# Performance work log

Measured on AMD Instinct MI355X. Metric: run time of the kernel, lower is better.

Reference implementation:

```python
import jax, jax.numpy as jnp
import numpy as np

WIN = 15
BINS = 32
ALPHA = 0.9
LAM1 = 0.5
LAM2 = 0.5


def _tmedian(x, axis):
    # torch-style median: k-th smallest with k=(n-1)//2 (lower middle), keepdims
    n = x.shape[axis]
    s = jnp.sort(x, axis=axis)
    return jnp.take(s, jnp.array([(n - 1) // 2]), axis=axis)


def _box_sum_1d(x, k, axis):
    # sliding-window sum (zero padding) via cumsum / integral image
    p = k // 2
    L = x.shape[axis]
    c = jnp.cumsum(x, axis=axis)
    pad = [(0, 0)] * x.ndim
    pad[axis] = (1, 0)
    c = jnp.pad(c, pad)
    i = jnp.arange(L)
    hi = jnp.clip(i + p + 1, 0, L)
    lo = jnp.clip(i - p, 0, L)
    return jnp.take(c, hi, axis=axis) - jnp.take(c, lo, axis=axis)


def _counts_1d(L, k, dtype):
    p = k // 2
    i = jnp.arange(L)
    return (jnp.clip(i + p + 1, 0, L) - jnp.clip(i - p, 0, L)).astype(dtype)


def box_avg(x, k):
    # avg_pool2d(stride=1, padding=k//2, count_include_pad=False) on [B,C,H,W]
    s = _box_sum_1d(_box_sum_1d(x, k, 2), k, 3)
    c = _counts_1d(x.shape[2], k, x.dtype)[:, None] * _counts_1d(x.shape[3], k, x.dtype)[None, :]
    return s / c


def avg3(x):
    # avg_pool2d(k=3, stride=1, pad=1, count_include_pad=True)
    return _box_sum_1d(_box_sum_1d(x, 3, 2), 3, 3) / 9.0


def _softplus(x):
    t = jnp.log1p(jnp.exp(-jnp.abs(x)))
    return jnp.where(x >= 0, x + t, t)


def _conv3(x, k):
    return jax.lax.conv_general_dilated(x, k, (1, 1), ((1, 1), (1, 1)),
                                        dimension_numbers=('NCHW', 'OIHW', 'NCHW'))


def _forward(lab, a_rand):
    B, _, H, W = lab.shape
    N = H * W
    f32 = lab.dtype
    L = lab[:, 0:1]
    a = lab[:, 1:2]
    b = lab[:, 2:3]
    kx = jnp.array([[-1, 0, 1], [-2, 0, 2], [-1, 0, 1]], f32).reshape(1, 1, 3, 3)
    ky = jnp.array([[-1, -2, -1], [0, 0, 0], [1, 2, 1]], f32).reshape(1, 1, 3, 3)
    gx = _conv3(L, kx)
    gy = _conv3(L, ky)
    E = avg3(gx * gx) + avg3(gy * gy)           # structure-tensor trace
    S = jnp.sqrt(a * a + b * b + 1e-8)           # chroma
    Xf = jnp.concatenate([E, S], 1).reshape(B, 2, N).transpose(0, 2, 1)   # [B,N,2]
    yf = L.reshape(B, 1, N).transpose(0, 2, 1)                            # [B,N,1]
    XtX = jnp.einsum('bni,bnj->bij', Xf, Xf)
    XtY = jnp.einsum('bni,bnj->bij', Xf, yf)
    beta = jnp.linalg.solve(XtX + 1e-6 * jnp.eye(2, dtype=f32), XtY)[..., 0]  # [B,2]
    pred = beta[:, 0][:, None, None, None] * E + beta[:, 1][:, None, None, None] * S
    L_perp = L - pred
    # robust scale + whitening of [L_perp, E, S]
    X3f = jnp.concatenate([L_perp, E, S], 1).reshape(B, 3, N).transpose(0, 2, 1)  # [B,N,3]
    med = _tmedian(X3f, 1)
    mad = _tmedian(jnp.abs(X3f - med), 1) * 1.4826 + 1e-8
    Xz = (X3f - med) / mad
    diff = Xz - Xz.mean(1, keepdims=True)
    cov = jnp.einsum('bni,bnj->bij', diff, diff) / N
    e, V = jnp.linalg.eigh(jnp.maximum(cov, 1e-8))
    Wwh = jnp.einsum('bij,bj,bkj->bik', V, 1.0 / jnp.sqrt(e), V)
    Xw = diff @ Wwh                                                       # [B,N,3]
    # 128-way random-projection kurtosis search
    an = a_rand / (jnp.linalg.norm(a_rand, axis=-1, keepdims=True) + 1e-12)
    z = jnp.einsum('bni,bti->bnt', Xw, an)                                # [B,N,128]
    zc = z - z.mean(1, keepdims=True)
    m2 = (zc ** 2).mean(1) + 1e-12
    m4 = (zc ** 4).mean(1)
    kurt = m4 / (m2 * m2) - 3.0
    best = jnp.argmax(jnp.abs(kurt), axis=1)
    a_star = jnp.take_along_axis(an, best[:, None, None], axis=1)[:, 0]   # [B,3]
    z_best = jnp.einsum('bni,bi->bn', Xw, a_star)                         # [B,N]
    # 1-D 2-component GMM, 10 EM steps
    K = 2
    q25 = jnp.quantile(z_best, 0.25, axis=1)
    q75 = jnp.quantile(z_best, 0.75, axis=1)
    mu = jnp.stack([q25, q75], 1)[:, None, :]   # [B,1,K]
    var = jnp.ones((B, 1, K), f32)
    pi = jnp.full((B, 1, K), 0.5, f32)
    x1 = z_best[:, :, None]                      # [B,N,1]
    R = jnp.zeros((B, N, K), f32)
    for _ in range(10):
        logp = (-0.5 * ((x1 - mu) ** 2 / (var + 1e-6))
                - 0.5 * jnp.log(var + 1e-6) + jnp.log(pi + 1e-8))
        R = jnp.exp(jax.nn.log_softmax(logp, axis=2))
        Nk = R.sum(1, keepdims=True)             # [B,1,K]
        mu = (R * x1).sum(1, keepdims=True) / (Nk + 1e-8)
        var = (R * (x1 - mu) ** 2).sum(1, keepdims=True) / (Nk + 1e-8) + 1e-6
        pi = Nk / N
    R_alpha = R ** ALPHA
    R_alpha = R_alpha / (R_alpha.sum(2, keepdims=True) + 1e-8)
    rk_maps = R_alpha.transpose(0, 2, 1).reshape(B, K, 1, H, W)
    # per-cluster weighted Mahalanobis distance in [L_perp,E,S] space
    eye3 = jnp.eye(3, dtype=f32)
    Dk = []
    for k in range(K):
        w = R_alpha[:, :, k]
        Wsum = w.sum(1, keepdims=True) + 1e-8
        mu_k = jnp.einsum('bn,bni->bi', w, X3f) / Wsum
        Xm = X3f - mu_k[:, None, :]
        cov_k = jnp.einsum('bn,bni,bnj->bij', w, Xm, Xm) / Wsum[..., None] + 1e-6 * eye3
        inv_k = jnp.linalg.inv(cov_k)
        Dk.append(jnp.sqrt(jnp.einsum('bni,bij,bnj->bn', Xm, inv_k, Xm) + 1e-8))
    Dk = jnp.stack(Dk, 2)                        # [B,N,K]
    Rtemp = jax.nn.softmax(jnp.log(R_alpha + 1e-8), axis=2)
    D_M = (Rtemp * Dk).sum(2).reshape(B, 1, H, W)
    # local luminance anomaly (box-filtered weighted mean/std)
    Z_LLA = []
    for k in range(K):
        rk = rk_maps[:, k]
        den = box_avg(rk, WIN) + 1e-8
        mu_b = box_avg(rk * L_perp, WIN) / den
        var_b = jnp.maximum(box_avg(rk * L_perp ** 2, WIN) / den - mu_b ** 2, 1e-8)
        lla = jnp.abs(L_perp - mu_b) / (jnp.sqrt(var_b) + 1e-8)
        v = lla.reshape(B, 1, N)
        mv = _tmedian(v, 2)
        mdv = _tmedian(jnp.abs(v - mv), 2) * 1.4826 + 1e-8
        Z_LLA.append(((v - mv) / mdv).reshape(B, 1, H, W))
    # global-vs-local histogram distance (GLD)
    Lmin = L_perp.min(axis=(2, 3), keepdims=True)
    Lmax = L_perp.max(axis=(2, 3), keepdims=True)
    Lnorm = jnp.clip((L_perp - Lmin) / (Lmax - Lmin + 1e-8), 0, 1)
    idx = jnp.clip((Lnorm * BINS).astype(jnp.int32), 0, BINS - 1)[:, 0]   # [B,H,W]
    onehot = jax.nn.one_hot(idx, BINS, dtype=f32).transpose(0, 3, 1, 2)   # [B,bins,H,W]
    Z_GLD = []
    for k in range(K):
        rk = rk_maps[:, k]
        w_hist = onehot * rk
        g_hist = w_hist.reshape(B, BINS, N).sum(-1)
        g_hist = g_hist / (g_hist.sum(1, keepdims=True) + 1e-8)
        g_cdf = jnp.cumsum(g_hist, 1)
        loc_cdf = jnp.cumsum(box_avg(w_hist, WIN), 1) / (box_avg(rk, WIN) + 1e-8)
        GLD = jnp.abs(loc_cdf - g_cdf[:, :, None, None]).sum(1) / BINS    # [B,H,W]
        v = GLD.reshape(B, N)
        mv = _tmedian(v, 1)                                              # [B,1]
        mdv = _tmedian(jnp.abs(v - mv), 1) * 1.4826 + 1e-8
        Z_GLD.append(((GLD - mv[:, :, None]) / mdv[:, :, None])[:, None])
    gamma = jnp.ones_like(L_perp)
    for k in range(K):
        gamma = gamma + rk_maps[:, k] * (LAM1 * _softplus(Z_LLA[k]) + LAM2 * _softplus(Z_GLD[k]))
    # structural decorrelation term over [E,S]
    ES = jnp.concatenate([E, S], 1).reshape(B, 2, N).transpose(0, 2, 1)
    med2 = _tmedian(ES, 1)
    mad2 = _tmedian(jnp.abs(ES - med2), 1) * 1.4826 + 1e-8
    ESz = (ES - med2) / mad2
    d = ESz - ESz.mean(1, keepdims=True)
    cov2 = jnp.einsum('bni,bnj->bij', d, d) / N + 1e-6 * jnp.eye(2, dtype=f32)
    inv2 = jnp.linalg.inv(cov2)
    d2 = jnp.einsum('bni,bij,bnj->bn', d, inv2, d).reshape(B, 1, H, W)
    R_struct = jnp.exp(-0.5 * d2)
    L_anom = jnp.maximum(D_M * gamma * (1.0 - R_struct), 0.0)
    flat = L_anom.reshape(B, -1)
    q1 = jnp.quantile(flat, 0.01, axis=1).reshape(B, 1, 1, 1)
    q9 = jnp.quantile(flat, 0.99, axis=1).reshape(B, 1, 1, 1)
    L_anom_norm = jnp.clip((L_anom - q1) / (q9 - q1 + 1e-8), 0, 1)
    return L_perp, L_anom_norm


def setup_inputs() -> dict:
    key = jax.random.key(0)
    k1, k2 = jax.random.split(key)
    return {
        'batch_lab_raw': jax.random.normal(k1, (2, 3, 384, 384), jnp.float32),
        'a_rand': jax.random.normal(k2, (2, 128, 3), jnp.float32),
    }


def reference(batch_lab_raw, a_rand):
    return _forward(batch_lab_raw, a_rand)
```

## Files before the change

kernel.cpp:

```cpp
#include <hip/hip_runtime.h>
#include <math.h>

#define HH 384
#define WW 384
#define NPIX (HH*WW)
#define NB 2
#define BN (NB*NPIX)
#define NT 128
#define NBINS 32
#define MEDRANK ((NPIX-1)/2)
#define RB 72
#define RB2 288
#define SEL_BLK 64
#define KDG 8
#define KSEG 16

#define A_BETA 0
#define A_XZ   16
#define A_ES   40
#define A_DK   56
#define A_GMM  128
#define A_ZTOT 272
#define A_GHIST 288
#define A_KURT 512

#define F_BETA 0
#define F_X3   8
#define F_MEAN 24
#define F_WWH  32
#define F_ASTAR 828
#define F_ZBQ  868
#define F_DKINV 880
#define F_CM   918
#define F_ESI  940
#define F_LAQ  952
#define F_GCDF 968
#define F_MMS_MIN 1280
#define F_MMS_MAX 1408


__device__ __forceinline__ double waveSum(double v){
#pragma unroll
  for(int o=32;o;o>>=1) v += __shfl_down(v,o,64);
  return v;
}
__device__ __forceinline__ unsigned f2u(float f){
  unsigned u = __float_as_uint(f);
  return (u & 0x80000000u) ? ~u : (u | 0x80000000u);
}
__device__ __forceinline__ float u2f(unsigned u){
  return __uint_as_float((u & 0x80000000u) ? (u ^ 0x80000000u) : ~u);
}
__device__ __forceinline__ float sp(float x){
  float t = log1pf(expf(-fabsf(x)));
  return x >= 0.f ? x + t : t;
}

struct SelBatch {
  const float* src[8];
  int rank[8];
  int fslot[8];
  int nt;
  int medmad;
};

__device__ void pickN(const unsigned* hp, int nb, int rank, unsigned& sel, int& nrank){
  __shared__ unsigned s_cum[256];
  __shared__ unsigned s_res[2];
  int tid = threadIdx.x;
  int base = tid*8;
  unsigned loc[8]; unsigned tsum=0;
#pragma unroll
  for(int j=0;j<8;j++){ unsigned v=(base+j<nb)?hp[base+j]:0u; loc[j]=v; tsum+=v; }
  s_cum[tid]=tsum;
  __syncthreads();
  for(int o=1;o<256;o<<=1){
    unsigned t=(tid>=o)?s_cum[tid-o]:0u;
    __syncthreads();
    s_cum[tid]+=t;
    __syncthreads();
  }
  unsigned cum=s_cum[tid], ex=cum-tsum;
  if(tsum>0u && (unsigned)rank>=ex && (unsigned)rank<cum){
    int rr=rank-(int)ex; unsigned bsel=0;
#pragma unroll
    for(int j=0;j<8;j++){ if((unsigned)rr<loc[j]){ bsel=(unsigned)(base+j); break; } rr-=(int)loc[j]; }
    s_res[0]=bsel; s_res[1]=(unsigned)rr;
  }
  __syncthreads();
  sel=s_res[0]; nrank=(int)s_res[1];
  __syncthreads();
}

__global__ void k_zero(double* A, float* F, unsigned* T, unsigned* H){
  int i = blockIdx.x*256 + threadIdx.x;
  if(i < 2048) A[i] = 0.0;
  if(i < 4096){
    unsigned* U = (unsigned*)F;
    unsigned v = 0u;
    if(i>=F_MMS_MIN && i<F_MMS_MIN+64) v = 0xFFFFFFFFu;
    U[i] = v;
  }
  if(i < 512) T[i] = 0u;
  for(int j=i; j<240*2048; j+=65536) H[j]=0u;
}

__global__ __launch_bounds__(256) void k_selp(SelBatch sb, unsigned* Hh, unsigned* T,
                                              float* F, int bid, int stage, int p){
  int task = blockIdx.x / SEL_BLK;
  int blk  = blockIdx.x % SEL_BLK;
  unsigned* meta = T + 384 + task*8;
  float center = (stage==1) ? __uint_as_float(meta[4]) : 0.f;
  unsigned pre = (p==2) ? 0u : meta[stage*2];
  __shared__ unsigned lh[2048];
  for(int j=threadIdx.x;j<2048;j+=256) lh[j]=0u;
  __syncthreads();
  const float* src = sb.src[task];
  for(int i=blk*256+threadIdx.x; i<NPIX; i+=SEL_BLK*256){
    float v = src[i];
    if(stage) v = fabsf(v-center);
    unsigned u = f2u(v);
    unsigned bin; bool ok;
    if(p==2){ bin = u>>21; ok = true; }
    else if(p==1){ bin = (u>>10)&2047u; ok = ((u>>21)==pre); }
    else { bin = u&1023u; ok = ((u>>10)==pre); }
    if(ok) atomicAdd(&lh[bin],1u);
  }
  __syncthreads();
  unsigned* hp = Hh + (size_t)(((bid*8+task)*2+stage)*3 + (2-p))*2048;
  for(int j=threadIdx.x;j<2048;j+=256){ unsigned c=lh[j]; if(c) atomicAdd(hp+j,c); }
  __shared__ int s_last;
  __syncthreads();
  if(threadIdx.x==0){
    __threadfence();
    s_last = (atomicAdd(&T[16+bid*64+task*8+stage*4+(2-p)],1u) == (unsigned)(SEL_BLK-1));
  }
  __syncthreads();
  if(!s_last) return;
  int r = (p==2) ? sb.rank[task] : (int)meta[stage*2+1];
  int nb = (p==0) ? 1024 : 2048;
  unsigned sel; int nr;
  pickN(hp, nb, r, sel, nr);
  if(threadIdx.x==0){
    if(p==2){ meta[stage*2]=sel; meta[stage*2+1]=(unsigned)nr; }
    else if(p==1){ meta[stage*2]=(pre<<11)|sel; meta[stage*2+1]=(unsigned)nr; }
    else {
      float val = u2f((pre<<10)|sel);
      if(stage==0){
        if(sb.medmad) meta[4]=__float_as_uint(val);
        else F[sb.fslot[task]]=val;
      } else {
        F[sb.fslot[task]]   = __uint_as_float(meta[4]);
        F[sb.fslot[task]+1] = val*1.4826f + 1e-8f;
      }
    }
  }
}

__device__ void quad_from_stats(double N0,double Sx0,double Sxx0,double Sxt,double Sxxt,
                                float& qa,float& qb,float& qc){
  double Nt=(double)NPIX;
  double N1=Nt-N0, Sx1=Sxt-Sx0, Sxx1=Sxxt-Sxx0;
  double mu0=Sx0/(N0+1e-8), mu1=Sx1/(N1+1e-8);
  double v0=(Sxx0-2.0*mu0*Sx0+mu0*mu0*N0)/(N0+1e-8)+1e-6;
  double v1=(Sxx1-2.0*mu1*Sx1+mu1*mu1*N1)/(N1+1e-8)+1e-6;
  double p0=N0/Nt, p1=N1/Nt;
  double c0=-0.5*log(v0+1e-6)+log(p0+1e-8);
  double c1=-0.5*log(v1+1e-6)+log(p1+1e-8);
  double iv0=0.5/(v0+1e-6), iv1=0.5/(v1+1e-6);
  qa=(float)(iv0-iv1);
  qb=(float)(2.0*(iv1*mu1-iv0*mu0));
  qc=(float)(iv0*mu0*mu0-iv1*mu1*mu1+c1-c0);
}
__device__ void quad_init(const float* F,int b,float& qa,float& qb,float& qc){
  const float* z = F + F_ZBQ + b*4;
  double h25 = 0.25*(double)(NPIX-1); double f25 = h25 - floor(h25);
  double h75 = 0.75*(double)(NPIX-1); double f75 = h75 - floor(h75);
  double mu0 = (double)z[0] + f25*((double)z[1]-(double)z[0]);
  double mu1 = (double)z[2] + f75*((double)z[3]-(double)z[2]);
  double iv = 0.5/(1.0+1e-6);
  qa = 0.f;
  qb = (float)(2.0*iv*(mu1-mu0));
  qc = (float)(iv*(mu0*mu0-mu1*mu1));
}

__global__ __launch_bounds__(256) void k_sobel(const float* lab, float* S, float* E){
  int bx = blockIdx.x % 24, by = (blockIdx.x/24) % 24, b = blockIdx.x/576;
  __shared__ float Lt[20][21];
  __shared__ float G[18][19];
  const float* Lb = lab + b*3*NPIX;
  int ox = bx*16, oy = by*16;
  for(int i=threadIdx.x; i<400; i+=256){
    int lx=i%20, ly=i/20;
    int gx_=ox-2+lx, gy_=oy-2+ly;
    Lt[ly][lx] = (gx_<0||gx_>=WW||gy_<0||gy_>=HH)?0.f:Lb[gy_*WW+gx_];
  }
  __syncthreads();
  for(int i=threadIdx.x; i<324; i+=256){
    int lx=i%18, ly=i/18;
    int px=lx+1, py=ly+1;
    int gxp=ox-2+px, gyp=oy-2+py;
    float g=0.f;
    if(gxp>=0&&gxp<WW&&gyp>=0&&gyp<HH){
      float gx = -Lt[py-1][px-1]+Lt[py-1][px+1] -2.f*Lt[py][px-1]+2.f*Lt[py][px+1] -Lt[py+1][px-1]+Lt[py+1][px+1];
      float gy = -Lt[py-1][px-1]-2.f*Lt[py-1][px]-Lt[py-1][px+1] +Lt[py+1][px-1]+2.f*Lt[py+1][px]+Lt[py+1][px+1];
      g = gx*gx+gy*gy;
    }
    G[ly][lx]=g;
  }
  __syncthreads();
  int tx = threadIdx.x%16, ty = threadIdx.x/16;
  float s=0;
#pragma unroll
  for(int dy=0;dy<3;dy++)
#pragma unroll
    for(int dx=0;dx<3;dx++) s += G[ty+dy][tx+dx];
  int n = (oy+ty)*WW + ox+tx;
  E[b*NPIX+n] = s*(1.f/9.f);
  float av=Lb[NPIX+n], bv=Lb[2*NPIX+n];
  S[b*NPIX+n] = sqrtf(av*av+bv*bv+1e-8f);
}

__global__ void k_beta_red(const float* E,const float* S,const float* lab,double* A,
                           float* F, unsigned* T){
  int b = blockIdx.x / RB, blk = blockIdx.x % RB;
  double s[5]={0,0,0,0,0};
  for(int n = blk*256 + threadIdx.x; n < NPIX; n += RB*256){
    float e=E[b*NPIX+n], ss=S[b*NPIX+n], l=lab[b*3*NPIX+n];
    s[0]+=(double)e*e; s[1]+=(double)e*ss; s[2]+=(double)ss*ss;
    s[3]+=(double)e*l; s[4]+=(double)ss*l;
  }
  __shared__ double red[4][5];
  int wave=threadIdx.x>>6, lane=threadIdx.x&63;
#pragma unroll
  for(int q=0;q<5;q++){
    s[q]=waveSum(s[q]);
    if(lane==0) red[wave][q]=s[q];
  }
  __syncthreads();
  if(threadIdx.x<5){
    double v = red[0][threadIdx.x]+red[1][threadIdx.x]+red[2][threadIdx.x]+red[3][threadIdx.x];
    atomicAdd(&A[A_BETA+b*5+threadIdx.x], v);
  }
  __shared__ int s_last;
  __syncthreads();
  if(threadIdx.x==0){
    __threadfence();
    s_last = (atomicAdd(&T[0],1u) == (unsigned)(NB*RB-1));
  }
  __syncthreads();
  if(!s_last || threadIdx.x) return;
  for(int bb=0;bb<NB;bb++){
    double EE=A[A_BETA+bb*5],ES=A[A_BETA+bb*5+1],SS=A[A_BETA+bb*5+2],EL=A[A_BETA+bb*5+3],SL=A[A_BETA+bb*5+4];
    double a00=EE+1e-6, a01=ES, a11=SS+1e-6;
    double det=a00*a11-a01*a01;
    F[F_BETA+bb*2]  =(float)(( a11*EL - a01*SL)/det);
    F[F_BETA+bb*2+1]=(float)((-a01*EL + a00*SL)/det);
  }
}

__global__ void k_lperp(const float* lab,const float* E,const float* S,const float* F,float* out0){
  int i = blockIdx.x*256 + threadIdx.x;
  int b=i/NPIX, n=i%NPIX;
  float v = lab[b*3*NPIX+n] - F[F_BETA+b*2]*E[i] - F[F_BETA+b*2+1]*S[i];
  out0[i] = v;
  unsigned u = f2u(v);
  unsigned mn=u, mx=u;
#pragma unroll
  for(int o=32;o;o>>=1){
    unsigned a = __shfl_down(mn,o,64); mn = (a<mn)?a:mn;
    unsigned c = __shfl_down(mx,o,64); mx = (c>mx)?c:mx;
  }
  __shared__ unsigned rmn[4], rmx[4];
  int wave=threadIdx.x>>6, lane=threadIdx.x&63;
  if(lane==0){ rmn[wave]=mn; rmx[wave]=mx; }
  __syncthreads();
  if(threadIdx.x==0){
    unsigned m0 = rmn[0]; unsigned m1 = rmx[0];
    for(int w=1;w<4;w++){ if(rmn[w]<m0)m0=rmn[w]; if(rmx[w]>m1)m1=rmx[w]; }
    unsigned* U = (unsigned*)F;
    int slot = blockIdx.x & 31;
    atomicMin(&U[F_MMS_MIN+b*32+slot], m0);
    atomicMax(&U[F_MMS_MAX+b*32+slot], m1);
  }
}

__global__ void k_xz_red(const float* Lp,const float* E,const float* S,float* F,double* A,
                         unsigned* T){
  int b = blockIdx.x / RB, blk = blockIdx.x % RB;
  const float* M = F + F_X3 + b*6;
  double s[9]={0,0,0,0,0,0,0,0,0};
  for(int n = blk*256 + threadIdx.x; n < NPIX; n += RB*256){
    float z0=(Lp[b*NPIX+n]-M[0])/M[1];
    float z1=(E [b*NPIX+n]-M[2])/M[3];
    float z2=(S [b*NPIX+n]-M[4])/M[5];
    s[0]+=z0; s[1]+=z1; s[2]+=z2;
    s[3]+=(double)z0*z0; s[4]+=(double)z0*z1; s[5]+=(double)z0*z2;
    s[6]+=(double)z1*z1; s[7]+=(double)z1*z2; s[8]+=(double)z2*z2;
  }
  __shared__ double red[4][9];
  int wave=threadIdx.x>>6, lane=threadIdx.x&63;
#pragma unroll
  for(int q=0;q<9;q++){
    s[q]=waveSum(s[q]);
    if(lane==0) red[wave][q]=s[q];
  }
  __syncthreads();
  if(threadIdx.x<9){
    double v = red[0][threadIdx.x]+red[1][threadIdx.x]+red[2][threadIdx.x]+red[3][threadIdx.x];
    atomicAdd(&A[A_XZ+b*9+threadIdx.x], v);
  }
  __shared__ int s_last;
  __syncthreads();
  if(threadIdx.x==0){
    __threadfence();
    s_last = (atomicAdd(&T[1],1u) == (unsigned)(NB*RB-1));
  }
  __syncthreads();
  if(!s_last) return;
  int bb = threadIdx.x;
  if(bb>=NB) return;
  const double* ss = A + A_XZ + bb*9;
  double inv = 1.0/(double)NPIX;
  double m0=ss[0]*inv, m1=ss[1]*inv, m2=ss[2]*inv;
  double a[3][3];
  a[0][0]=fmax(ss[3]*inv-m0*m0,1e-8);
  a[0][1]=a[1][0]=fmax(ss[4]*inv-m0*m1,1e-8);
  a[0][2]=a[2][0]=fmax(ss[5]*inv-m0*m2,1e-8);
  a[1][1]=fmax(ss[6]*inv-m1*m1,1e-8);
  a[1][2]=a[2][1]=fmax(ss[7]*inv-m1*m2,1e-8);
  a[2][2]=fmax(ss[8]*inv-m2*m2,1e-8);
  double V[3][3]={{1,0,0},{0,1,0},{0,0,1}};
  for(int sweep=0;sweep<40;sweep++){
    for(int pp=0;pp<3;pp++){
      int p = (pp==2)?1:0;
      int q = (pp==0)?1:2;
      double apq=a[p][q];
      if(fabs(apq)<1e-30) continue;
      double theta=(a[q][q]-a[p][p])/(2.0*apq);
      double t=((theta>=0)?1.0:-1.0)/(fabs(theta)+sqrt(1.0+theta*theta));
      double c=1.0/sqrt(1.0+t*t), sn=t*c;
      for(int k2=0;k2<3;k2++){ double akp=a[k2][p],akq=a[k2][q];
        a[k2][p]=c*akp-sn*akq; a[k2][q]=sn*akp+c*akq; }
      for(int k2=0;k2<3;k2++){ double apk=a[p][k2],aqk=a[q][k2];
        a[p][k2]=c*apk-sn*aqk; a[q][k2]=sn*apk+c*aqk; }
      for(int k2=0;k2<3;k2++){ double vkp=V[k2][p],vkq=V[k2][q];
        V[k2][p]=c*vkp-sn*vkq; V[k2][q]=sn*vkp+c*vkq; }
    }
  }
  double is0=1.0/sqrt(a[0][0]), is1=1.0/sqrt(a[1][1]), is2=1.0/sqrt(a[2][2]);
  for(int i=0;i<3;i++) for(int j=0;j<3;j++){
    double w = V[i][0]*is0*V[j][0] + V[i][1]*is1*V[j][1] + V[i][2]*is2*V[j][2];
    F[F_WWH + bb*9 + i*3 + j] = (float)w;
  }
  F[F_MEAN+bb*3]=(float)m0; F[F_MEAN+bb*3+1]=(float)m1; F[F_MEAN+bb*3+2]=(float)m2;
}

__global__ void k_xw(const float* Lp,const float* E,const float* S,const float* F,
                     float* Xw,int* idxP){
  __shared__ float s_mn, s_mx;
  int i = blockIdx.x*256 + threadIdx.x;
  int b=i/NPIX;
  if(threadIdx.x==0){
    const unsigned* U = (const unsigned*)F;
    unsigned mn=0xFFFFFFFFu, mx=0u;
    for(int s2=0;s2<32;s2++){
      unsigned a=U[F_MMS_MIN+b*32+s2]; if(a<mn)mn=a;
      unsigned c=U[F_MMS_MAX+b*32+s2]; if(c>mx)mx=c;
    }
    s_mn=u2f(mn); s_mx=u2f(mx);
  }
  __syncthreads();
  const float* M = F + F_X3 + b*6;
  float lp = Lp[i];
  float z0=(lp-M[0])/M[1];
  float z1=(E [i]-M[2])/M[3];
  float z2=(S [i]-M[4])/M[5];
  float d0=z0-F[F_MEAN+b*3], d1=z1-F[F_MEAN+b*3+1], d2=z2-F[F_MEAN+b*3+2];
  const float* Wm = F + F_WWH + b*9;
  Xw[3*(size_t)i  ]=d0*Wm[0]+d1*Wm[3]+d2*Wm[6];
  Xw[3*(size_t)i+1]=d0*Wm[1]+d1*Wm[4]+d2*Wm[7];
  Xw[3*(size_t)i+2]=d0*Wm[2]+d1*Wm[5]+d2*Wm[8];
  float ln = (lp-s_mn)/(s_mx-s_mn+1e-8f);
  ln = fminf(fmaxf(ln,0.f),1.f);
  int id = (int)(ln*32.f);
  idxP[i] = id>31?31:(id<0?0:id);
}

__global__ __launch_bounds__(256) void k_kurt(const float* Xw, const float* arand,
                                              double* A, float* F, unsigned* T){
  int g = blockIdx.x;
  int b   = g / ((NT/KDG)*KSEG);
  int rem = g % ((NT/KDG)*KSEG);
  int dg  = rem / KSEG;
  int seg = rem % KSEG;
  float a0[KDG],a1[KDG],a2[KDG];
#pragma unroll
  for(int j=0;j<KDG;j++){
    const float* ar = arand + (b*NT+dg*KDG+j)*3;
    float q0=ar[0],q1=ar[1],q2=ar[2];
    float nrm=(float)(sqrt((double)q0*q0+(double)q1*q1+(double)q2*q2)+1e-12);
    a0[j]=q0/nrm; a1[j]=q1/nrm; a2[j]=q2/nrm;
  }
  const float* X = Xw + (size_t)b*NPIX*3;
  double s[KDG][4];
#pragma unroll
  for(int j=0;j<KDG;j++){ s[j][0]=0; s[j][1]=0; s[j][2]=0; s[j][3]=0; }
  const int cnt = NPIX/KSEG;
  int start = seg*cnt;
  for(int n=start+threadIdx.x; n<start+cnt; n+=256){
    const float* p = X + 3*(size_t)n;
    float x=p[0], y=p[1], z=p[2];
#pragma unroll
    for(int j=0;j<KDG;j++){
      float zz = fmaf(x,a0[j],fmaf(y,a1[j], z*a2[j]));
      float z2f = zz*zz;
      s[j][0]+=zz; s[j][1]+=z2f; s[j][2]+=z2f*zz; s[j][3]+=(double)z2f*z2f;
    }
  }
  __shared__ double red[4][KDG*4];
  int wave=threadIdx.x>>6, lane=threadIdx.x&63;
#pragma unroll
  for(int j=0;j<KDG;j++)
#pragma unroll
    for(int m=0;m<4;m++){
      double v=waveSum(s[j][m]);
      if(lane==0) red[wave][j*4+m]=v;
    }
  __syncthreads();
  if(threadIdx.x<KDG*4){
    double v = red[0][threadIdx.x]+red[1][threadIdx.x]+red[2][threadIdx.x]+red[3][threadIdx.x];
    int j=threadIdx.x>>2, m=threadIdx.x&3;
    atomicAdd(&A[A_KURT + (size_t)(b*NT+dg*KDG+j)*4 + m], v);
  }
  __shared__ int s_last;
  __syncthreads();
  if(threadIdx.x==0){
    __threadfence();
    s_last = (atomicAdd(&T[5],1u) == (unsigned)(NB*(NT/KDG)*KSEG-1));
  }
  __syncthreads();
  if(!s_last) return;
  __shared__ float ak[NB*NT];
  {
    int tid=threadIdx.x;
    const double* K = A + A_KURT + (size_t)tid*4;
    double inv=1.0/(double)NPIX;
    double mean=K[0]*inv, M2=K[1]*inv, M3=K[2]*inv, M4=K[3]*inv;
    double m2 = M2 - mean*mean + 1e-12;
    double m4 = M4 - 4.0*mean*M3 + 6.0*mean*mean*M2 - 3.0*mean*mean*mean*mean;
    ak[tid] = (float)fabs(m4/(m2*m2) - 3.0);
  }
  __syncthreads();
  if(threadIdx.x<NB){
    int bb=threadIdx.x;
    int best=0; float bv=ak[bb*NT];
    for(int j=1;j<NT;j++){ float v=ak[bb*NT+j]; if(v>bv){bv=v;best=j;} }
    const float* ar = arand + (bb*NT+best)*3;
    double nrm = sqrt((double)ar[0]*ar[0]+(double)ar[1]*ar[1]+(double)ar[2]*ar[2])+1e-12;
    F[F_ASTAR+bb*3]  =(float)(ar[0]/nrm);
    F[F_ASTAR+bb*3+1]=(float)(ar[1]/nrm);
    F[F_ASTAR+bb*3+2]=(float)(ar[2]/nrm);
  }
}

__global__ void k_zbest(const float* Xw,const float* F,float* zb,double* A){
  int i = blockIdx.x*256 + threadIdx.x;
  int b=i/NPIX;
  const float* p = Xw + 3*(size_t)i;
  float v = p[0]*F[F_ASTAR+b*3] + p[1]*F[F_ASTAR+b*3+1] + p[2]*F[F_ASTAR+b*3+2];
  zb[i]=v;
  double s0=waveSum((double)v), s1=waveSum((double)v*v);
  __shared__ double red[4][2];
  int wave=threadIdx.x>>6, lane=threadIdx.x&63;
  if(lane==0){ red[wave][0]=s0; red[wave][1]=s1; }
  __syncthreads();
  if(threadIdx.x<2){
    double v2 = red[0][threadIdx.x]+red[1][threadIdx.x]+red[2][threadIdx.x]+red[3][threadIdx.x];
    atomicAdd(&A[A_ZTOT+b*2+threadIdx.x], v2);
  }
}

__global__ __launch_bounds__(256) void k_gmm_red(const float* zb, const float* F, double* A, int it){
  __shared__ float Q[3];
  __shared__ double red[4][3];
  int b = blockIdx.x / RB2, blk = blockIdx.x % RB2;
  if(threadIdx.x==0){
    float qa,qb,qc;
    if(it==0) quad_init(F,b,qa,qb,qc);
    else {
      const double* g = A + A_GMM + (it-1)*8 + b*4;
      quad_from_stats(g[0],g[1],g[2],A[A_ZTOT+b*2],A[A_ZTOT+b*2+1],qa,qb,qc);
    }
    Q[0]=qa;Q[1]=qb;Q[2]=qc;
  }
  __syncthreads();
  float qa=Q[0],qb=Q[1],qc=Q[2];
  double s0=0,s1=0,s2=0;
  for(int n = blk*256 + threadIdx.x; n < NPIX; n += RB2*256){
    float x = zb[b*NPIX+n];
    float f = fmaf(fmaf(qa,x,qb),x,qc);
    float r0 = 1.f/(1.f+expf(f));
    float rx = r0*x;
    s0+=r0; s1+=rx; s2+=(double)rx*x;
  }
  int wave=threadIdx.x>>6, lane=threadIdx.x&63;
  s0=waveSum(s0); s1=waveSum(s1); s2=waveSum(s2);
  if(lane==0){ red[wave][0]=s0; red[wave][1]=s1; red[wave][2]=s2; }
  __syncthreads();
  if(threadIdx.x<3){
    double v = red[0][threadIdx.x]+red[1][threadIdx.x]+red[2][threadIdx.x]+red[3][threadIdx.x];
    atomicAdd(&A[A_GMM+it*8+b*4+threadIdx.x], v);
  }
}

__global__ void k_ralpha(const float* zb, float* F, double* A, const int* idxP,
                         float* Ra0, float* Ra1, unsigned* T){
  __shared__ float h0[NBINS], h1[NBINS];
  __shared__ float Q[3];
  if(threadIdx.x<NBINS){ h0[threadIdx.x]=0.f; h1[threadIdx.x]=0.f; }
  int i = blockIdx.x*256 + threadIdx.x;
  int b=i/NPIX;
  if(threadIdx.x==0){
    const double* g = A + A_GMM + 8*8 + b*4;
    float qa,qb,qc;
    quad_from_stats(g[0],g[1],g[2],A[A_ZTOT+b*2],A[A_ZTOT+b*2+1],qa,qb,qc);
    Q[0]=qa;Q[1]=qb;Q[2]=qc;
  }
  __syncthreads();
  float x = zb[i];
  float f = fmaf(fmaf(Q[0],x,Q[1]),x,Q[2]);
  float r0 = 1.f/(1.f+expf(f));
  float r1 = 1.f-r0;
  float ra0=powf(r0,0.9f), ra1=powf(r1,0.9f);
  float s=ra0+ra1+1e-8f;
  ra0/=s; ra1/=s;
  Ra0[i]=ra0; Ra1[i]=ra1;
  int id = idxP[i];
  atomicAdd(&h0[id], ra0);
  atomicAdd(&h1[id], ra1);
  __syncthreads();
  if(threadIdx.x<NBINS){
    if(h0[threadIdx.x]!=0.f) atomicAdd(&A[A_GHIST+(0*NB+b)*32+threadIdx.x], (double)h0[threadIdx.x]);
    if(h1[threadIdx.x]!=0.f) atomicAdd(&A[A_GHIST+(1*NB+b)*32+threadIdx.x], (double)h1[threadIdx.x]);
  }
  __shared__ int s_last;
  __syncthreads();
  if(threadIdx.x==0){
    __threadfence();
    s_last = (atomicAdd(&T[2],1u) == (unsigned)(BN/256-1));
  }
  __syncthreads();
  if(!s_last) return;
  int t = threadIdx.x;
  if(t>=4) return;
  const double* gh = A + A_GHIST + t*32;
  double sum=0;
  for(int j=0;j<NBINS;j++) sum += gh[j];
  double c=0;
  for(int j=0;j<NBINS;j++){
    c += gh[j]/(sum+1e-8);
    F[F_GCDF+t*32+j]=(float)c;
  }
}

__global__ void k_dk_red(const float* Lp,const float* E,const float* S,
                         const float* Ra0,const float* Ra1,double* A,float* F,unsigned* T){
  int b = blockIdx.x / RB, blk = blockIdx.x % RB;
  double s[20];
#pragma unroll
  for(int q=0;q<20;q++) s[q]=0;
  for(int n = blk*256 + threadIdx.x; n < NPIX; n += RB*256){
    int i=b*NPIX+n;
    double w0=Ra0[i], w1=Ra1[i];
    double x0=Lp[i], x1=E[i], x2=S[i];
    s[0]+=w0; s[1]+=w0*x0; s[2]+=w0*x1; s[3]+=w0*x2;
    s[4]+=w0*x0*x0; s[5]+=w0*x0*x1; s[6]+=w0*x0*x2; s[7]+=w0*x1*x1; s[8]+=w0*x1*x2; s[9]+=w0*x2*x2;
    s[10]+=w1; s[11]+=w1*x0; s[12]+=w1*x1; s[13]+=w1*x2;
    s[14]+=w1*x0*x0; s[15]+=w1*x0*x1; s[16]+=w1*x0*x2; s[17]+=w1*x1*x1; s[18]+=w1*x1*x2; s[19]+=w1*x2*x2;
  }
  __shared__ double red[4][20];
  int wave=threadIdx.x>>6, lane=threadIdx.x&63;
#pragma unroll
  for(int q=0;q<20;q++){
    s[q]=waveSum(s[q]);
    if(lane==0) red[wave][q]=s[q];
  }
  __syncthreads();
  if(threadIdx.x<20){
    double v = red[0][threadIdx.x]+red[1][threadIdx.x]+red[2][threadIdx.x]+red[3][threadIdx.x];
    atomicAdd(&A[A_DK+b*20+threadIdx.x], v);
  }
  __shared__ int s_last;
  __syncthreads();
  if(threadIdx.x==0){
    __threadfence();
    s_last = (atomicAdd(&T[3],1u) == (unsigned)(NB*RB-1));
  }
  __syncthreads();
  if(!s_last || threadIdx.x) return;
  for(int bb=0;bb<NB;bb++) for(int k=0;k<2;k++){
    const double* ss = A + A_DK + (bb*2+k)*10;
    double W0=ss[0], Ws=W0+1e-8;
    double mu0=ss[1]/Ws, mu1=ss[2]/Ws, mu2=ss[3]/Ws;
    double C00=(ss[4]-2.0*mu0*ss[1]+mu0*mu0*W0)/Ws + 1e-6;
    double C01=(ss[5]-mu0*ss[2]-mu1*ss[1]+mu0*mu1*W0)/Ws;
    double C02=(ss[6]-mu0*ss[3]-mu2*ss[1]+mu0*mu2*W0)/Ws;
    double C11=(ss[7]-2.0*mu1*ss[2]+mu1*mu1*W0)/Ws + 1e-6;
    double C12=(ss[8]-mu1*ss[3]-mu2*ss[2]+mu1*mu2*W0)/Ws;
    double C22=(ss[9]-2.0*mu2*ss[3]+mu2*mu2*W0)/Ws + 1e-6;
    double det = C00*(C11*C22-C12*C12) - C01*(C01*C22-C12*C02) + C02*(C01*C12-C11*C02);
    double id = 1.0/det;
    float* P = F + F_DKINV + (bb*2+k)*9;
    P[0]=(float)((C11*C22-C12*C12)*id);
    P[1]=(float)((C02*C12-C01*C22)*id);
    P[2]=(float)((C01*C12-C02*C11)*id);
    P[3]=(float)((C00*C22-C02*C02)*id);
    P[4]=(float)((C01*C02-C00*C12)*id);
    P[5]=(float)((C00*C11-C01*C01)*id);
    P[6]=(float)mu0; P[7]=(float)mu1; P[8]=(float)mu2;
  }
}
__global__ void k_dm(const float* Lp,const float* E,const float* S,
                     const float* Ra0,const float* Ra1,const float* F,float* DM){
  int i = blockIdx.x*256 + threadIdx.x; if(i>=BN) return;
  int b=i/NPIX;
  float x0=Lp[i], x1=E[i], x2=S[i];
  float D[2];
#pragma unroll
  for(int k=0;k<2;k++){
    const float* P = F + F_DKINV + (b*2+k)*9;
    float d0=x0-P[6], d1=x1-P[7], d2=x2-P[8];
    float q = d0*d0*P[0] + d1*d1*P[3] + d2*d2*P[5]
            + 2.f*(d0*d1*P[1] + d0*d2*P[2] + d1*d2*P[4]);
    D[k]=sqrtf(q+1e-8f);
  }
  float w0=Ra0[i]+1e-8f, w1=Ra1[i]+1e-8f;
  DM[i] = (w0*D[0]+w1*D[1])/(w0+w1);
}

__global__ __launch_bounds__(256) void k_lla(const float* Ra0, const float* Ra1,
                                             const float* Lp, float* tmpL){
  int kk = blockIdx.x / (NB*576);
  int inner = blockIdx.x % (NB*576);
  int bx = inner % 24, by = (inner/24) % 24, b = inner/576;
  const float* rk = kk ? Ra1 : Ra0;
  __shared__ float Rt[30][31], Lt[30][31];
  __shared__ float h0[30][17], h1[30][17], h2[30][17];
  int ox = bx*16, oy = by*16;
  const float* Rb = rk + (size_t)b*NPIX;
  const float* Lb = Lp + (size_t)b*NPIX;
  for(int i=threadIdx.x; i<900; i+=256){
    int lx=i%30, ly=i/30;
    int gx_=ox-7+lx, gy_=oy-7+ly;
    bool in = (gx_>=0&&gx_<WW&&gy_>=0&&gy_<HH);
    Rt[ly][lx]= in ? Rb[gy_*WW+gx_] : 0.f;
    Lt[ly][lx]= in ? Lb[gy_*WW+gx_] : 0.f;
  }
  __syncthreads();
  for(int i=threadIdx.x; i<480; i+=256){
    int j=i%16, r=i/16;
    float s0=0,s1=0,s2=0;
#pragma unroll
    for(int d=0;d<15;d++){
      float rr=Rt[r][j+d], ll=Lt[r][j+d];
      s0+=rr; float rl=rr*ll; s1+=rl; s2+=rl*ll;
    }
    h0[r][j]=s0; h1[r][j]=s1; h2[r][j]=s2;
  }
  __syncthreads();
  int tx=threadIdx.x%16, ty=threadIdx.x/16;
  float S0=0,S1=0,S2=0;
#pragma unroll
  for(int d=0;d<15;d++){ S0+=h0[ty+d][tx]; S1+=h1[ty+d][tx]; S2+=h2[ty+d][tx]; }
  int x=ox+tx, y=oy+ty;
  float cy = (float)((y+8<HH?y+8:HH)-(y-7>0?y-7:0));
  float cx = (float)((x+8<WW?x+8:WW)-(x-7>0?x-7:0));
  float cnt = cy*cx;
  float den = S0/cnt + 1e-8f;
  float mu  = (S1/cnt)/den;
  float var = fmaxf((S2/cnt)/den - mu*mu, 1e-8f);
  int n = y*WW+x;
  tmpL[(size_t)kk*BN + b*NPIX+n] = fabsf(Lb[n]-mu)/(sqrtf(var)+1e-8f);
}

__global__ __launch_bounds__(256) void k_gldf(const float* Ra0, const float* Ra1,
                                              const int* idxP, const float* F, float* tmpG){
  int kk = blockIdx.x / (NB*576);
  int inner = blockIdx.x % (NB*576);
  int bx = inner % 24, by = (inner/24) % 24, b = inner/576;
  const float* rk = kk ? Ra1 : Ra0;
  __shared__ float Rt[30][31];
  __shared__ unsigned char It[30][32];
  __shared__ float Hh[32*480];
  __shared__ float gc[NBINS];
  if(threadIdx.x<NBINS) gc[threadIdx.x]=F[F_GCDF+(kk*NB+b)*32+threadIdx.x];
  int ox=bx*16, oy=by*16;
  const float* Rb = rk + (size_t)b*NPIX;
  const int* Ib = idxP + (size_t)b*NPIX;
  for(int i=threadIdx.x;i<900;i+=256){
    int lx=i%30, ly=i/30;
    int gx_=ox-7+lx, gy_=oy-7+ly;
    bool in = (gx_>=0&&gx_<WW&&gy_>=0&&gy_<HH);
    Rt[ly][lx] = in? Rb[gy_*WW+gx_] : 0.f;
    It[ly][lx] = in? (unsigned char)Ib[gy_*WW+gx_] : 0;
  }
  for(int i=threadIdx.x;i<32*480;i+=256) Hh[i]=0.f;
  __syncthreads();
  for(int i=threadIdx.x;i<480;i+=256){
    int j=i%16, r=i/16;
    for(int d=0;d<15;d++) Hh[(int)It[r][j+d]*480 + i] += Rt[r][j+d];
  }
  __syncthreads();
  int tx=threadIdx.x%16, ty=threadIdx.x/16;
  float vs[32];
  float tot=0;
#pragma unroll
  for(int bin=0;bin<NBINS;bin++){
    float s=0;
#pragma unroll
    for(int d=0;d<15;d++) s += Hh[bin*480 + (ty+d)*16+tx];
    vs[bin]=s; tot+=s;
  }
  int x=ox+tx, y=oy+ty;
  float cy = (float)((y+8<HH?y+8:HH)-(y-7>0?y-7:0));
  float cx = (float)((x+8<WW?x+8:WW)-(x-7>0?x-7:0));
  float cnt = cy*cx;
  float den = tot/cnt + 1e-8f;
  float cs=0, acc=0;
#pragma unroll
  for(int bin=0;bin<NBINS;bin++){
    cs += vs[bin];
    acc += fabsf((cs/cnt)/den - gc[bin]);
  }
  tmpG[(size_t)kk*BN + b*NPIX + y*WW + x] = acc*(1.f/32.f);
}

__global__ void k_gamma(const float* tmpL,const float* tmpG,const float* Ra0,const float* Ra1,
                        const float* F,float* gamma){
  int i = blockIdx.x*256 + threadIdx.x; if(i>=BN) return;
  int b=i/NPIX;
  float g = 1.0f;
#pragma unroll
  for(int kk=0;kk<2;kk++){
    const float* ML = F + F_CM + (kk*4 + 0 + b)*2;
    const float* MG = F + F_CM + (kk*4 + 2 + b)*2;
    float zl=(tmpL[(size_t)kk*BN+i]-ML[0])/ML[1];
    float zg=(tmpG[(size_t)kk*BN+i]-MG[0])/MG[1];
    float rk = kk ? Ra1[i] : Ra0[i];
    g += rk*(0.5f*sp(zl)+0.5f*sp(zg));
  }
  gamma[i] = g;
}

__global__ void k_es_red(const float* E,const float* S,float* F,double* A,unsigned* T){
  int b = blockIdx.x / RB, blk = blockIdx.x % RB;
  const float* M = F + F_X3 + b*6;
  double s[5]={0,0,0,0,0};
  for(int n = blk*256 + threadIdx.x; n < NPIX; n += RB*256){
    float z0=(E[b*NPIX+n]-M[2])/M[3];
    float z1=(S[b*NPIX+n]-M[4])/M[5];
    s[0]+=z0; s[1]+=z1; s[2]+=(double)z0*z0; s[3]+=(double)z0*z1; s[4]+=(double)z1*z1;
  }
  __shared__ double red[4][5];
  int wave=threadIdx.x>>6, lane=threadIdx.x&63;
#pragma unroll
  for(int q=0;q<5;q++){
    s[q]=waveSum(s[q]);
    if(lane==0) red[wave][q]=s[q];
  }
  __syncthreads();
  if(threadIdx.x<5){
    double v = red[0][threadIdx.x]+red[1][threadIdx.x]+red[2][threadIdx.x]+red[3][threadIdx.x];
    atomicAdd(&A[A_ES+b*5+threadIdx.x], v);
  }
  __shared__ int s_last;
  __syncthreads();
  if(threadIdx.x==0){
    __threadfence();
    s_last = (atomicAdd(&T[4],1u) == (unsigned)(NB*RB-1));
  }
  __syncthreads();
  if(!s_last || threadIdx.x) return;
  for(int bb=0;bb<NB;bb++){
    const double* ss = A + A_ES + bb*5;
    double inv=1.0/(double)NPIX;
    double m0=ss[0]*inv, m1=ss[1]*inv;
    double c00=ss[2]*inv - m0*m0 + 1e-6;
    double c01=ss[3]*inv - m0*m1;
    double c11=ss[4]*inv - m1*m1 + 1e-6;
    double det=c00*c11-c01*c01;
    float* P = F + F_ESI + bb*5;
    P[0]=(float)m0; P[1]=(float)m1;
    P[2]=(float)(c11/det); P[3]=(float)(-c01/det); P[4]=(float)(c00/det);
  }
}
__global__ void k_lanom(const float* E,const float* S,const float* DM,const float* gamma,
                        const float* F,float* La){
  int i = blockIdx.x*256 + threadIdx.x; if(i>=BN) return;
  int b=i/NPIX;
  const float* M = F + F_X3 + b*6;
  const float* P = F + F_ESI + b*5;
  float z0=(E[i]-M[2])/M[3];
  float z1=(S[i]-M[4])/M[5];
  float d0=z0-P[0], d1=z1-P[1];
  float d2 = d0*d0*P[2] + 2.f*d0*d1*P[3] + d1*d1*P[4];
  float Rs = expf(-0.5f*d2);
  La[i] = fmaxf(DM[i]*gamma[i]*(1.f-Rs), 0.f);
}
__global__ void k_out2(const float* La, const float* F, float* out){
  int i = blockIdx.x*256 + threadIdx.x; if(i>=BN) return;
  int b=i/NPIX;
  const float* v = F + F_LAQ + b*4;
  double h1 = 0.01*(double)(NPIX-1); double f1 = h1 - floor(h1);
  double h9 = 0.99*(double)(NPIX-1); double f9 = h9 - floor(h9);
  float q1 = (float)((double)v[0] + f1*((double)v[1]-(double)v[0]));
  float q9 = (float)((double)v[2] + f9*((double)v[3]-(double)v[2]));
  float r = (La[i]-q1)/(q9-q1+1e-8f);
  out[BN + i] = fminf(fmaxf(r,0.f),1.f);
}

static void run_sel(const SelBatch& sb, unsigned* H, unsigned* T, float* F, int bid, hipStream_t s){
  for(int p=2;p>=0;--p) k_selp<<<sb.nt*SEL_BLK,256,0,s>>>(sb,H,T,F,bid,0,p);
  if(sb.medmad) for(int p=2;p>=0;--p) k_selp<<<sb.nt*SEL_BLK,256,0,s>>>(sb,H,T,F,bid,1,p);
}

extern "C" void kernel_launch(void* const* d_in, const int* in_sizes, int n_in,
                              void* d_out, int out_size, void* d_ws, size_t ws_size,
                              hipStream_t stream){
  (void)in_sizes; (void)n_in; (void)out_size; (void)ws_size;
  const float* lab   = (const float*)d_in[0];
  const float* arand = (const float*)d_in[1];
  float* out = (float*)d_out;
  char* wsb = (char*)d_ws;
  double* A = (double*)wsb;
  float*  F = (float*)(wsb + 16384);
  unsigned* T = (unsigned*)(wsb + 32768);
  unsigned* H = (unsigned*)(wsb + 65536);
  float* planes = (float*)(wsb + (size_t)4*1024*1024);
  float* E    = planes;
  float* S    = planes + (size_t)BN;
  float* tA   = planes + (size_t)2*BN;
  float* tmpL = planes + (size_t)3*BN;
  float* tmpG = planes + (size_t)5*BN;
  float* Xw   = planes + (size_t)7*BN;
  float* zb   = planes + (size_t)10*BN;
  float* Ra0  = planes + (size_t)11*BN;
  float* Ra1  = planes + (size_t)12*BN;
  float* DM   = planes + (size_t)13*BN;
  float* gamma= planes + (size_t)14*BN;
  int*   idxP = (int*)(planes + (size_t)16*BN);

  const int GBN = BN/256;

  k_zero<<<256,256,0,stream>>>(A,F,T,H);
  k_sobel<<<NB*576,256,0,stream>>>(lab,S,E);
  k_beta_red<<<NB*RB,256,0,stream>>>(E,S,lab,A,F,T);
  k_lperp<<<GBN,256,0,stream>>>(lab,E,S,F,out);

  SelBatch sbX; sbX.nt=6; sbX.medmad=1;
  for(int b=0;b<NB;b++){
    sbX.src[b*3+0]=out+(size_t)b*NPIX; sbX.src[b*3+1]=E+(size_t)b*NPIX; sbX.src[b*3+2]=S+(size_t)b*NPIX;
    for(int ch=0;ch<3;ch++){ sbX.rank[b*3+ch]=MEDRANK; sbX.fslot[b*3+ch]=F_X3+(b*3+ch)*2; }
  }
  run_sel(sbX,H,T,F,0,stream);

  k_xz_red<<<NB*RB,256,0,stream>>>(out,E,S,F,A,T);
  k_xw<<<GBN,256,0,stream>>>(out,E,S,F,Xw,idxP);
  k_kurt<<<NB*(NT/KDG)*KSEG,256,0,stream>>>(Xw,arand,A,F,T);
  k_zbest<<<GBN,256,0,stream>>>(Xw,F,zb,A);

  SelBatch sbZ; sbZ.nt=8; sbZ.medmad=0;
  {
    int rr[4]={36863,36864,110591,110592};
    for(int b=0;b<NB;b++) for(int ri=0;ri<4;ri++){
      int t=b*4+ri;
      sbZ.src[t]=zb+(size_t)b*NPIX; sbZ.rank[t]=rr[ri]; sbZ.fslot[t]=F_ZBQ+b*4+ri;
    }
  }
  run_sel(sbZ,H,T,F,1,stream);

  for(int it=0; it<9; ++it)
    k_gmm_red<<<NB*RB2,256,0,stream>>>(zb,F,A,it);
  k_ralpha<<<GBN,256,0,stream>>>(zb,F,A,idxP,Ra0,Ra1,T);
  k_dk_red<<<NB*RB,256,0,stream>>>(out,E,S,Ra0,Ra1,A,F,T);
  k_dm<<<GBN,256,0,stream>>>(out,E,S,Ra0,Ra1,F,DM);

  k_lla<<<2*NB*576,256,0,stream>>>(Ra0,Ra1,out,tmpL);
  k_gldf<<<2*NB*576,256,0,stream>>>(Ra0,Ra1,idxP,F,tmpG);

  SelBatch sbC; sbC.nt=8; sbC.medmad=1;
  for(int kk=0;kk<2;kk++) for(int isG=0;isG<2;isG++) for(int b=0;b<NB;b++){
    int t = kk*4 + isG*2 + b;
    sbC.src[t] = (isG? tmpG: tmpL) + (size_t)kk*BN + (size_t)b*NPIX;
    sbC.rank[t]=MEDRANK; sbC.fslot[t]=F_CM + t*2;
  }
  run_sel(sbC,H,T,F,2,stream);

  k_gamma<<<GBN,256,0,stream>>>(tmpL,tmpG,Ra0,Ra1,F,gamma);

  k_es_red<<<NB*RB,256,0,stream>>>(E,S,F,A,T);
  k_lanom<<<GBN,256,0,stream>>>(E,S,DM,gamma,F,tA);

  SelBatch sbL; sbL.nt=8; sbL.medmad=0;
  {
    int rr[4]={1474,1475,145980,145981};
    for(int b=0;b<NB;b++) for(int ri=0;ri<4;ri++){
      int t=b*4+ri;
      sbL.src[t]=tA+(size_t)b*NPIX; sbL.rank[t]=rr[ri]; sbL.fslot[t]=F_LAQ+b*4+ri;
    }
  }
  run_sel(sbL,H,T,F,3,stream);

  k_out2<<<GBN,256,0,stream>>>(tA,F,out);
}
```

Before: 642.1 us.

## Fuse DM, gamma and anomaly kernels; split GLD histogram into halves with sliding sums

Three per-pixel elementwise kernels (k_dm, k_gamma, k_lanom) are merged into one kernel, so the DM and gamma intermediate planes are never written to or read back from global memory. k_es_red moves earlier in the launch sequence; it only depends on E, S and the medians. k_gldf now builds the local histogram in two halves of 16 bins each, which halves its shared-memory footprint and should allow more resident blocks. Each half uses a sliding-window vertical sum instead of 15 reads per bin per pixel, at the cost of extra syncs and a second pass over the tile.

```diff
diff --git a/kernel.cpp b/kernel.cpp
--- a/kernel.cpp
+++ b/kernel.cpp
@@ -14,6 +14,8 @@
 #define SEL_BLK 64
 #define KDG 8
 #define KSEG 16
+#define GHS 496
+#define GVS 272
 
 #define A_BETA 0
 #define A_XZ   16
@@ -37,7 +39,6 @@
 #define F_GCDF 968
 #define F_MMS_MIN 1280
 #define F_MMS_MAX 1408
-
 
 __device__ __forceinline__ double waveSum(double v){
 #pragma unroll
@@ -621,23 +622,6 @@
     P[6]=(float)mu0; P[7]=(float)mu1; P[8]=(float)mu2;
   }
 }
-__global__ void k_dm(const float* Lp,const float* E,const float* S,
-                     const float* Ra0,const float* Ra1,const float* F,float* DM){
-  int i = blockIdx.x*256 + threadIdx.x; if(i>=BN) return;
-  int b=i/NPIX;
-  float x0=Lp[i], x1=E[i], x2=S[i];
-  float D[2];
-#pragma unroll
-  for(int k=0;k<2;k++){
-    const float* P = F + F_DKINV + (b*2+k)*9;
-    float d0=x0-P[6], d1=x1-P[7], d2=x2-P[8];
-    float q = d0*d0*P[0] + d1*d1*P[3] + d2*d2*P[5]
-            + 2.f*(d0*d1*P[1] + d0*d2*P[2] + d1*d2*P[4]);
-    D[k]=sqrtf(q+1e-8f);
-  }
-  float w0=Ra0[i]+1e-8f, w1=Ra1[i]+1e-8f;
-  DM[i] = (w0*D[0]+w1*D[1])/(w0+w1);
-}
 
 __global__ __launch_bounds__(256) void k_lla(const float* Ra0, const float* Ra1,
                                              const float* Lp, float* tmpL){
@@ -692,7 +676,8 @@
   const float* rk = kk ? Ra1 : Ra0;
   __shared__ float Rt[30][31];
   __shared__ unsigned char It[30][32];
-  __shared__ float Hh[32*480];
+  __shared__ float Hh[16*GHS];
+  __shared__ float Vv[16*GVS];
   __shared__ float gc[NBINS];
   if(threadIdx.x<NBINS) gc[threadIdx.x]=F[F_GCDF+(kk*NB+b)*32+threadIdx.x];
   int ox=bx*16, oy=by*16;
@@ -705,27 +690,45 @@
     Rt[ly][lx] = in? Rb[gy_*WW+gx_] : 0.f;
     It[ly][lx] = in? (unsigned char)Ib[gy_*WW+gx_] : 0;
   }
-  for(int i=threadIdx.x;i<32*480;i+=256) Hh[i]=0.f;
-  __syncthreads();
-  for(int i=threadIdx.x;i<480;i+=256){
-    int j=i%16, r=i/16;
-    for(int d=0;d<15;d++) Hh[(int)It[r][j+d]*480 + i] += Rt[r][j+d];
-  }
-  __syncthreads();
   int tx=threadIdx.x%16, ty=threadIdx.x/16;
   float vs[32];
-  float tot=0;
-#pragma unroll
-  for(int bin=0;bin<NBINS;bin++){
-    float s=0;
-#pragma unroll
-    for(int d=0;d<15;d++) s += Hh[bin*480 + (ty+d)*16+tx];
-    vs[bin]=s; tot+=s;
+  for(int half=0; half<2; ++half){
+    int base = half*16;
+    __syncthreads();
+    for(int i=threadIdx.x;i<16*GHS;i+=256) Hh[i]=0.f;
+    __syncthreads();
+    for(int i=threadIdx.x;i<480;i+=256){
+      int j=i%16, r=i/16;
+      for(int d=0;d<15;d++){
+        int bin = (int)It[r][j+d];
+        if((bin>>4)==half) Hh[(bin&15)*GHS + i] += Rt[r][j+d];
+      }
+    }
+    __syncthreads();
+    {
+      int j  = threadIdx.x%16;
+      int bn = threadIdx.x/16;
+      const float* h = Hh + bn*GHS;
+      float s=0;
+#pragma unroll
+      for(int r=0;r<15;r++) s += h[r*16+j];
+      Vv[bn*GVS + 0*16 + j] = s;
+      for(int yy=1;yy<16;yy++){
+        s += h[(yy+14)*16+j] - h[(yy-1)*16+j];
+        Vv[bn*GVS + yy*16 + j] = s;
+      }
+    }
+    __syncthreads();
+#pragma unroll
+    for(int jb=0;jb<16;jb++) vs[base+jb] = Vv[jb*GVS + ty*16 + tx];
   }
   int x=ox+tx, y=oy+ty;
   float cy = (float)((y+8<HH?y+8:HH)-(y-7>0?y-7:0));
   float cx = (float)((x+8<WW?x+8:WW)-(x-7>0?x-7:0));
   float cnt = cy*cx;
+  float tot=0;
+#pragma unroll
+  for(int bin=0;bin<NBINS;bin++) tot += vs[bin];
   float den = tot/cnt + 1e-8f;
   float cs=0, acc=0;
 #pragma unroll
@@ -736,10 +739,25 @@
   tmpG[(size_t)kk*BN + b*NPIX + y*WW + x] = acc*(1.f/32.f);
 }
 
-__global__ void k_gamma(const float* tmpL,const float* tmpG,const float* Ra0,const float* Ra1,
-                        const float* F,float* gamma){
+__global__ void k_lanom(const float* Lp,const float* E,const float* S,
+                        const float* tmpL,const float* tmpG,
+                        const float* Ra0,const float* Ra1,
+                        const float* F,float* La){
   int i = blockIdx.x*256 + threadIdx.x; if(i>=BN) return;
   int b=i/NPIX;
+  float x0=Lp[i], x1=E[i], x2=S[i];
+  float D[2];
+#pragma unroll
+  for(int k=0;k<2;k++){
+    const float* P = F + F_DKINV + (b*2+k)*9;
+    float d0=x0-P[6], d1=x1-P[7], d2=x2-P[8];
+    float q = d0*d0*P[0] + d1*d1*P[3] + d2*d2*P[5]
+            + 2.f*(d0*d1*P[1] + d0*d2*P[2] + d1*d2*P[4]);
+    D[k]=sqrtf(q+1e-8f);
+  }
+  float ra0=Ra0[i], ra1=Ra1[i];
+  float w0=ra0+1e-8f, w1=ra1+1e-8f;
+  float DM = (w0*D[0]+w1*D[1])/(w0+w1);
   float g = 1.0f;
 #pragma unroll
   for(int kk=0;kk<2;kk++){
@@ -747,10 +765,17 @@
     const float* MG = F + F_CM + (kk*4 + 2 + b)*2;
     float zl=(tmpL[(size_t)kk*BN+i]-ML[0])/ML[1];
     float zg=(tmpG[(size_t)kk*BN+i]-MG[0])/MG[1];
-    float rk = kk ? Ra1[i] : Ra0[i];
+    float rk = kk ? ra1 : ra0;
     g += rk*(0.5f*sp(zl)+0.5f*sp(zg));
   }
-  gamma[i] = g;
+  const float* M = F + F_X3 + b*6;
+  const float* P = F + F_ESI + b*5;
+  float z0=(x1-M[2])/M[3];
+  float z1=(x2-M[4])/M[5];
+  float d0=z0-P[0], d1=z1-P[1];
+  float d2 = d0*d0*P[2] + 2.f*d0*d1*P[3] + d1*d1*P[4];
+  float Rs = expf(-0.5f*d2);
+  La[i] = fmaxf(DM*g*(1.f-Rs), 0.f);
 }
 
 __global__ void k_es_red(const float* E,const float* S,float* F,double* A,unsigned* T){
@@ -794,19 +819,6 @@
     P[0]=(float)m0; P[1]=(float)m1;
     P[2]=(float)(c11/det); P[3]=(float)(-c01/det); P[4]=(float)(c00/det);
   }
-}
-__global__ void k_lanom(const float* E,const float* S,const float* DM,const float* gamma,
-                        const float* F,float* La){
-  int i = blockIdx.x*256 + threadIdx.x; if(i>=BN) return;
-  int b=i/NPIX;
-  const float* M = F + F_X3 + b*6;
-  const float* P = F + F_ESI + b*5;
-  float z0=(E[i]-M[2])/M[3];
-  float z1=(S[i]-M[4])/M[5];
-  float d0=z0-P[0], d1=z1-P[1];
-  float d2 = d0*d0*P[2] + 2.f*d0*d1*P[3] + d1*d1*P[4];
-  float Rs = expf(-0.5f*d2);
-  La[i] = fmaxf(DM[i]*gamma[i]*(1.f-Rs), 0.f);
 }
 __global__ void k_out2(const float* La, const float* F, float* out){
   int i = blockIdx.x*256 + threadIdx.x; if(i>=BN) return;
@@ -847,8 +859,6 @@
   float* zb   = planes + (size_t)10*BN;
   float* Ra0  = planes + (size_t)11*BN;
   float* Ra1  = planes + (size_t)12*BN;
-  float* DM   = planes + (size_t)13*BN;
-  float* gamma= planes + (size_t)14*BN;
   int*   idxP = (int*)(planes + (size_t)16*BN);
 
   const int GBN = BN/256;
@@ -866,6 +876,7 @@
   run_sel(sbX,H,T,F,0,stream);
 
   k_xz_red<<<NB*RB,256,0,stream>>>(out,E,S,F,A,T);
+  k_es_red<<<NB*RB,256,0,stream>>>(E,S,F,A,T);
   k_xw<<<GBN,256,0,stream>>>(out,E,S,F,Xw,idxP);
   k_kurt<<<NB*(NT/KDG)*KSEG,256,0,stream>>>(Xw,arand,A,F,T);
   k_zbest<<<GBN,256,0,stream>>>(Xw,F,zb,A);
@@ -884,7 +895,6 @@
     k_gmm_red<<<NB*RB2,256,0,stream>>>(zb,F,A,it);
   k_ralpha<<<GBN,256,0,stream>>>(zb,F,A,idxP,Ra0,Ra1,T);
   k_dk_red<<<NB*RB,256,0,stream>>>(out,E,S,Ra0,Ra1,A,F,T);
-  k_dm<<<GBN,256,0,stream>>>(out,E,S,Ra0,Ra1,F,DM);
 
   k_lla<<<2*NB*576,256,0,stream>>>(Ra0,Ra1,out,tmpL);
   k_gldf<<<2*NB*576,256,0,stream>>>(Ra0,Ra1,idxP,F,tmpG);
@@ -897,10 +907,7 @@
   }
   run_sel(sbC,H,T,F,2,stream);
 
-  k_gamma<<<GBN,256,0,stream>>>(tmpL,tmpG,Ra0,Ra1,F,gamma);
-
-  k_es_red<<<NB*RB,256,0,stream>>>(E,S,F,A,T);
-  k_lanom<<<GBN,256,0,stream>>>(E,S,DM,gamma,F,tA);
+  k_lanom<<<GBN,256,0,stream>>>(out,E,S,tmpL,tmpG,Ra0,Ra1,F,tA);
 
   SelBatch sbL; sbL.nt=8; sbL.medmad=0;
   {
```

Measured after the change: 647.8 us. No clear change (+0.9%).
